# Performance work log

Hardware: AMD Instinct MI355X
Metric: run time of the kernel (lower is better)

Reference implementation:

```python
import jax, jax.numpy as jnp
import numpy as np

N_NODES = 100000
N_EDGES = 3200000
BATCH = 16
LAYER_NUMBER = 4


def setup_inputs() -> dict:
    key = jax.random.key(0)
    k1, k2, k3, k4 = jax.random.split(key, 4)
    x = jax.random.normal(k1, (N_NODES, BATCH), dtype=jnp.float32)
    # learnable per-edge weights (log1p(counts) at init in the original; the
    # parameter itself is what is learned, so a plain random init is faithful)
    weights = jax.random.normal(k2, (N_EDGES,), dtype=jnp.float32)
    row = jax.random.randint(k3, (N_EDGES,), 0, N_NODES, dtype=jnp.int64)
    col = jax.random.randint(k4, (N_EDGES,), 0, N_NODES, dtype=jnp.int64)
    return {"x": x, "weights": weights, "row": row, "col": col}


def reference(x, weights, row, col):
    # Repeated sparse COO SpMM: y <- A @ y, applied layer_number times,
    # where A[row[e], col[e]] = weights[e].
    def step(y, _):
        msg = weights[:, None] * y[col]                      # [E, B] gather + scale
        y_new = jax.ops.segment_sum(msg, row, num_segments=N_NODES)  # [N, B] scatter-add
        return y_new, None

    y, _ = jax.lax.scan(step, x, None, length=LAYER_NUMBER)
    return y
```

## Files before the change

### kernel.cpp

```cpp
#include <hip/hip_runtime.h>

#define N_NODES 100000
#define N_EDGES 3200000
#define BATCH 16
#define BKT_SHIFT 6
#define BKT_NODES 64
#define K_BUCKETS 1563
#define NB 256
#define SUB (N_EDGES / NB)
#define FT 512
#define SCAN_T 256
#define SCAN_C 7
#define CAP 4096

__global__ void hist_kernel(const int* __restrict__ row, int* __restrict__ blk_cnt) {
    __shared__ int lh[K_BUCKETS];
    int t = threadIdx.x, blk = blockIdx.x;
    for (int k = t; k < K_BUCKETS; k += 256) lh[k] = 0;
    __syncthreads();
    int base = blk * SUB;
    for (int e = base + t; e < base + SUB; e += 256)
        atomicAdd(&lh[row[e] >> BKT_SHIFT], 1);
    __syncthreads();
    for (int k = t; k < K_BUCKETS; k += 256)
        blk_cnt[k * NB + blk] = lh[k];
}

__global__ void colscan_kernel(int* __restrict__ blk_cnt, int* __restrict__ totals) {
    int bkt = blockIdx.x * blockDim.x + threadIdx.x;
    if (bkt >= K_BUCKETS) return;
    int4* p = (int4*)&blk_cnt[bkt * NB];
    int acc = 0;
    for (int q = 0; q < NB / 4; q++) {
        int4 v = p[q];
        int4 o;
        o.x = acc; acc += v.x;
        o.y = acc; acc += v.y;
        o.z = acc; acc += v.z;
        o.w = acc; acc += v.w;
        p[q] = o;
    }
    totals[bkt] = acc;
}

__global__ void scan_kernel(const int* __restrict__ totals, int* __restrict__ bptr,
                            int* __restrict__ row_ptr) {
    __shared__ int s[SCAN_T];
    int t = threadIdx.x;
    int loc[SCAN_C];
    int sum = 0;
    for (int i = 0; i < SCAN_C; i++) {
        int idx = t * SCAN_C + i;
        int v = (idx < K_BUCKETS) ? totals[idx] : 0;
        loc[i] = v;
        sum += v;
    }
    s[t] = sum;
    __syncthreads();
    for (int off = 1; off < SCAN_T; off <<= 1) {
        int x = (t >= off) ? s[t - off] : 0;
        __syncthreads();
        s[t] += x;
        __syncthreads();
    }
    int excl = s[t] - sum;
    for (int i = 0; i < SCAN_C; i++) {
        int idx = t * SCAN_C + i;
        if (idx < K_BUCKETS) bptr[idx] = excl;
        excl += loc[i];
    }
    if (t == 0) { bptr[K_BUCKETS] = N_EDGES; row_ptr[N_NODES] = N_EDGES; }
}

__global__ void __launch_bounds__(FT) fill_kernel(
        const int* __restrict__ row, const int* __restrict__ col,
        const float* __restrict__ w,
        const int* __restrict__ bptr, const int* __restrict__ blk_cnt,
        uint2* __restrict__ entries) {
    __shared__ uint2 sbuf[SUB];
    __shared__ int lbeg[K_BUCKETS];
    __shared__ int lcur[K_BUCKETS];
    __shared__ int sscan[FT];
    int t = threadIdx.x, blk = blockIdx.x;
    for (int k = t; k < K_BUCKETS; k += FT) lcur[k] = 0;
    __syncthreads();
    int base = blk * SUB;
    for (int e = base + t; e < base + SUB; e += FT)
        atomicAdd(&lcur[row[e] >> BKT_SHIFT], 1);
    __syncthreads();
    int loc[4];
    int sum = 0;
    #pragma unroll
    for (int j = 0; j < 4; j++) {
        int k = t * 4 + j;
        int v = (k < K_BUCKETS) ? lcur[k] : 0;
        loc[j] = v;
        sum += v;
    }
    sscan[t] = sum;
    __syncthreads();
    for (int off = 1; off < FT; off <<= 1) {
        int x = (t >= off) ? sscan[t - off] : 0;
        __syncthreads();
        sscan[t] += x;
        __syncthreads();
    }
    int excl = sscan[t] - sum;
    #pragma unroll
    for (int j = 0; j < 4; j++) {
        int k = t * 4 + j;
        if (k < K_BUCKETS) { lbeg[k] = excl; lcur[k] = excl; }
        excl += loc[j];
    }
    __syncthreads();
    for (int e = base + t; e < base + SUB; e += FT) {
        int r = row[e];
        int bkt = r >> BKT_SHIFT;
        int pos = atomicAdd(&lcur[bkt], 1);
        sbuf[pos] = make_uint2(((unsigned)(r & (BKT_NODES - 1)) << 17) | (unsigned)col[e],
                               __float_as_uint(w[e]));
    }
    __syncthreads();
    int lane = t & 7;
    for (int k = (t >> 3); k < K_BUCKETS; k += FT / 8) {
        int lb = lbeg[k];
        int le = lcur[k];
        int dst = bptr[k] + blk_cnt[k * NB + blk];
        for (int i = lb + lane; i < le; i += 8)
            entries[dst + (i - lb)] = sbuf[i];
    }
}

__global__ void nodesort_kernel(const int* __restrict__ bptr, uint2* __restrict__ entries,
                                int* __restrict__ row_ptr) {
    __shared__ uint2 ebuf[CAP];
    __shared__ int nh[BKT_NODES];
    __shared__ int nc[BKT_NODES];
    int t = threadIdx.x, b = blockIdx.x;
    int beg = bptr[b], end = bptr[b + 1];
    int n = min(end - beg, CAP);
    if (t < BKT_NODES) nh[t] = 0;
    __syncthreads();
    for (int k = t; k < n; k += 256) {
        uint2 r = entries[beg + k];
        ebuf[k] = r;
        atomicAdd(&nh[r.x >> 17], 1);
    }
    __syncthreads();
    if (t == 0) {
        int acc = 0;
        for (int i = 0; i < BKT_NODES; i++) {
            int v = nh[i];
            int node = b * BKT_NODES + i;
            if (node < N_NODES) row_ptr[node] = beg + acc;
            nc[i] = acc;
            acc += v;
        }
    }
    __syncthreads();
    for (int k = t; k < n; k += 256) {
        uint2 r = ebuf[k];
        int pos = atomicAdd(&nc[r.x >> 17], 1);
        entries[beg + pos] = r;
    }
}

__global__ void __launch_bounds__(256) pull_kernel(const float* __restrict__ y,
                            const uint2* __restrict__ entries,
                            const int* __restrict__ row_ptr,
                            float* __restrict__ out) {
    int tid = blockIdx.x * blockDim.x + threadIdx.x;
    int node = tid >> 2;
    int q = tid & 3;
    if (node >= N_NODES) return;
    int beg = row_ptr[node];
    int end = row_ptr[node + 1];
    float4 acc = make_float4(0.f, 0.f, 0.f, 0.f);
    if (beg < end) {
        int lim = end - 1;
        uint2 r[8];
        #pragma unroll
        for (int j = 0; j < 8; j++) r[j] = entries[min(beg + j, lim)];
        int i = beg;
        while (i + 8 <= end) {
            float4 yv[8];
            #pragma unroll
            for (int j = 0; j < 8; j++)
                yv[j] = *(const float4*)&y[(r[j].x & 0x1FFFFu) * BATCH + q * 4];
            uint2 nx[8];
            #pragma unroll
            for (int j = 0; j < 8; j++)
                nx[j] = entries[min(i + 8 + j, lim)];
            #pragma unroll
            for (int j = 0; j < 8; j++) {
                float wj = __uint_as_float(r[j].y);
                acc.x += wj * yv[j].x;
                acc.y += wj * yv[j].y;
                acc.z += wj * yv[j].z;
                acc.w += wj * yv[j].w;
            }
            #pragma unroll
            for (int j = 0; j < 8; j++) r[j] = nx[j];
            i += 8;
        }
        if (i < end) {
            float4 yv[8];
            #pragma unroll
            for (int j = 0; j < 8; j++)
                yv[j] = *(const float4*)&y[(r[j].x & 0x1FFFFu) * BATCH + q * 4];
            #pragma unroll
            for (int j = 0; j < 8; j++)
                if (i + j < end) {
                    float wj = __uint_as_float(r[j].y);
                    acc.x += wj * yv[j].x;
                    acc.y += wj * yv[j].y;
                    acc.z += wj * yv[j].z;
                    acc.w += wj * yv[j].w;
                }
        }
    }
    *(float4*)&out[node * BATCH + q * 4] = acc;
}

extern "C" void kernel_launch(void* const* d_in, const int* in_sizes, int n_in,
                              void* d_out, int out_size, void* d_ws, size_t ws_size,
                              hipStream_t stream) {
    const float* x   = (const float*)d_in[0];
    const float* w   = (const float*)d_in[1];
    const int*   row = (const int*)d_in[2];
    const int*   col = (const int*)d_in[3];
    float*       out = (float*)d_out;

    char* p = (char*)d_ws;
    uint2* entries = (uint2*)p;  p += (size_t)N_EDGES * sizeof(uint2);
    float* buf     = (float*)p;
    int*   blk_cnt = (int*)buf;
    p += (size_t)N_NODES * BATCH * sizeof(float);
    int* totals  = (int*)p;      p += 8192;
    int* bptr    = (int*)p;      p += 8192;
    int* row_ptr = (int*)p;

    hist_kernel<<<NB, 256, 0, stream>>>(row, blk_cnt);
    colscan_kernel<<<(K_BUCKETS + 255) / 256, 256, 0, stream>>>(blk_cnt, totals);
    scan_kernel<<<1, SCAN_T, 0, stream>>>(totals, bptr, row_ptr);
    fill_kernel<<<NB, FT, 0, stream>>>(row, col, w, bptr, blk_cnt, entries);
    nodesort_kernel<<<K_BUCKETS, 256, 0, stream>>>(bptr, entries, row_ptr);

    const int pgrid = (N_NODES * 4 + 255) / 256;
    pull_kernel<<<pgrid, 256, 0, stream>>>(x,   entries, row_ptr, buf);
    pull_kernel<<<pgrid, 256, 0, stream>>>(buf, entries, row_ptr, out);
    pull_kernel<<<pgrid, 256, 0, stream>>>(out, entries, row_ptr, buf);
    pull_kernel<<<pgrid, 256, 0, stream>>>(buf, entries, row_ptr, out);
}
```

Measured before the change: 357.9 us.

## Split feature batch into two half-width planes for cache-resident SpMM gathers

Adds a split kernel that rearranges x into two planar halves of 8 features each. Each layer then runs two pull passes, one per half, with 2 threads per node instead of 4. Halving the gathered vector table is meant to let the random y[col] gathers stay in on-chip cache. The cost is streaming the sorted edge entries twice per layer, plus one extra kernel launch per layer and a split pass; the last layer writes back in the interleaved output layout.

```diff
diff --git a/kernel.cpp b/kernel.cpp
--- a/kernel.cpp
+++ b/kernel.cpp
@@ -165,14 +165,28 @@
     }
 }
 
-__global__ void __launch_bounds__(256) pull_kernel(const float* __restrict__ y,
-                            const uint2* __restrict__ entries,
-                            const int* __restrict__ row_ptr,
-                            float* __restrict__ out) {
+__global__ void split_kernel(const float* __restrict__ x, float* __restrict__ planes) {
+    int node = blockIdx.x * blockDim.x + threadIdx.x;
+    if (node >= N_NODES) return;
+    const float4* src = (const float4*)&x[node * BATCH];
+    float4 a0 = src[0], a1 = src[1], a2 = src[2], a3 = src[3];
+    float4* p0 = (float4*)&planes[(size_t)node * 8];
+    p0[0] = a0; p0[1] = a1;
+    float4* p1 = (float4*)&planes[(size_t)N_NODES * 8 + (size_t)node * 8];
+    p1[0] = a2; p1[1] = a3;
+}
+
+__global__ void __launch_bounds__(256) pull_half_kernel(
+        const float* __restrict__ yplanes,
+        const uint2* __restrict__ entries,
+        const int* __restrict__ row_ptr,
+        float* __restrict__ out,
+        int half, int out_interleaved) {
     int tid = blockIdx.x * blockDim.x + threadIdx.x;
-    int node = tid >> 2;
-    int q = tid & 3;
+    int node = tid >> 1;
+    int q = tid & 1;
     if (node >= N_NODES) return;
+    const float* in = yplanes + (size_t)half * N_NODES * 8 + q * 4;
     int beg = row_ptr[node];
     int end = row_ptr[node + 1];
     float4 acc = make_float4(0.f, 0.f, 0.f, 0.f);
@@ -186,7 +200,7 @@
             float4 yv[8];
             #pragma unroll
             for (int j = 0; j < 8; j++)
-                yv[j] = *(const float4*)&y[(r[j].x & 0x1FFFFu) * BATCH + q * 4];
+                yv[j] = *(const float4*)&in[(r[j].x & 0x1FFFFu) * 8];
             uint2 nx[8];
             #pragma unroll
             for (int j = 0; j < 8; j++)
@@ -207,7 +221,7 @@
             float4 yv[8];
             #pragma unroll
             for (int j = 0; j < 8; j++)
-                yv[j] = *(const float4*)&y[(r[j].x & 0x1FFFFu) * BATCH + q * 4];
+                yv[j] = *(const float4*)&in[(r[j].x & 0x1FFFFu) * 8];
             #pragma unroll
             for (int j = 0; j < 8; j++)
                 if (i + j < end) {
@@ -219,7 +233,10 @@
                 }
         }
     }
-    *(float4*)&out[node * BATCH + q * 4] = acc;
+    size_t dst = out_interleaved
+        ? (size_t)node * BATCH + half * 8 + q * 4
+        : (size_t)half * N_NODES * 8 + (size_t)node * 8 + q * 4;
+    *(float4*)&out[dst] = acc;
 }
 
 extern "C" void kernel_launch(void* const* d_in, const int* in_sizes, int n_in,
@@ -246,9 +263,15 @@
     fill_kernel<<<NB, FT, 0, stream>>>(row, col, w, bptr, blk_cnt, entries);
     nodesort_kernel<<<K_BUCKETS, 256, 0, stream>>>(bptr, entries, row_ptr);
 
-    const int pgrid = (N_NODES * 4 + 255) / 256;
-    pull_kernel<<<pgrid, 256, 0, stream>>>(x,   entries, row_ptr, buf);
-    pull_kernel<<<pgrid, 256, 0, stream>>>(buf, entries, row_ptr, out);
-    pull_kernel<<<pgrid, 256, 0, stream>>>(out, entries, row_ptr, buf);
-    pull_kernel<<<pgrid, 256, 0, stream>>>(buf, entries, row_ptr, out);
-}
+    split_kernel<<<(N_NODES + 255) / 256, 256, 0, stream>>>(x, out);
+
+    const int pgrid = (N_NODES * 2 + 255) / 256;
+    pull_half_kernel<<<pgrid, 256, 0, stream>>>(out, entries, row_ptr, buf, 0, 0);
+    pull_half_kernel<<<pgrid, 256, 0, stream>>>(out, entries, row_ptr, buf, 1, 0);
+    pull_half_kernel<<<pgrid, 256, 0, stream>>>(buf, entries, row_ptr, out, 0, 0);
+    pull_half_kernel<<<pgrid, 256, 0, stream>>>(buf, entries, row_ptr, out, 1, 0);
+    pull_half_kernel<<<pgrid, 256, 0, stream>>>(out, entries, row_ptr, buf, 0, 0);
+    pull_half_kernel<<<pgrid, 256, 0, stream>>>(out, entries, row_ptr, buf, 1, 0);
+    pull_half_kernel<<<pgrid, 256, 0, stream>>>(buf, entries, row_ptr, out, 0, 1);
+    pull_half_kernel<<<pgrid, 256, 0, stream>>>(buf, entries, row_ptr, out, 1, 1);
+}
```

New measurement: 487.2 us. 36.1% more time.

## Double partition blocks and scan bucket counts with one wavefront per bucket

Applied to the files above, without the earlier changes.

Doubles the number of edge-partition blocks in the histogram and fill stages so each block handles half as many edges, giving more blocks to spread across CUs. The per-bucket column scan now uses a 64-lane wavefront with shuffle-based prefix sums instead of one serial thread per bucket, which matters more now that each column is twice as long. The fill copy-out uses 4 lanes per bucket instead of 8 to match the smaller per-bucket chunk sizes. The cost is a larger count matrix and more scattered, smaller copy segments.

```diff
diff --git a/kernel.cpp b/kernel.cpp
--- a/kernel.cpp
+++ b/kernel.cpp
@@ -6,7 +6,7 @@
 #define BKT_SHIFT 6
 #define BKT_NODES 64
 #define K_BUCKETS 1563
-#define NB 256
+#define NB 512
 #define SUB (N_EDGES / NB)
 #define FT 512
 #define SCAN_T 256
@@ -27,20 +27,33 @@
 }
 
 __global__ void colscan_kernel(int* __restrict__ blk_cnt, int* __restrict__ totals) {
-    int bkt = blockIdx.x * blockDim.x + threadIdx.x;
-    if (bkt >= K_BUCKETS) return;
-    int4* p = (int4*)&blk_cnt[bkt * NB];
-    int acc = 0;
-    for (int q = 0; q < NB / 4; q++) {
-        int4 v = p[q];
-        int4 o;
-        o.x = acc; acc += v.x;
-        o.y = acc; acc += v.y;
-        o.z = acc; acc += v.z;
-        o.w = acc; acc += v.w;
-        p[q] = o;
-    }
-    totals[bkt] = acc;
+    int wid = (blockIdx.x * blockDim.x + threadIdx.x) >> 6;
+    int lane = threadIdx.x & 63;
+    if (wid >= K_BUCKETS) return;
+    int* p = &blk_cnt[wid * NB + lane * 8];
+    int4 a = ((int4*)p)[0];
+    int4 b = ((int4*)p)[1];
+    int lt = a.x + a.y + a.z + a.w + b.x + b.y + b.z + b.w;
+    int pref = lt;
+    #pragma unroll
+    for (int off = 1; off < 64; off <<= 1) {
+        int v = __shfl_up(pref, off, 64);
+        if (lane >= off) pref += v;
+    }
+    int run = pref - lt;
+    int4 oa, ob;
+    oa.x = run; run += a.x;
+    oa.y = run; run += a.y;
+    oa.z = run; run += a.z;
+    oa.w = run; run += a.w;
+    ob.x = run; run += b.x;
+    ob.y = run; run += b.y;
+    ob.z = run; run += b.z;
+    ob.w = run; run += b.w;
+    ((int4*)p)[0] = oa;
+    ((int4*)p)[1] = ob;
+    int tot = __shfl(pref, 63, 64);
+    if (lane == 0) totals[wid] = tot;
 }
 
 __global__ void scan_kernel(const int* __restrict__ totals, int* __restrict__ bptr,
@@ -121,12 +134,12 @@
                                __float_as_uint(w[e]));
     }
     __syncthreads();
-    int lane = t & 7;
-    for (int k = (t >> 3); k < K_BUCKETS; k += FT / 8) {
+    int lane = t & 3;
+    for (int k = (t >> 2); k < K_BUCKETS; k += FT / 4) {
         int lb = lbeg[k];
         int le = lcur[k];
         int dst = bptr[k] + blk_cnt[k * NB + blk];
-        for (int i = lb + lane; i < le; i += 8)
+        for (int i = lb + lane; i < le; i += 4)
             entries[dst + (i - lb)] = sbuf[i];
     }
 }
@@ -241,7 +254,7 @@
     int* row_ptr = (int*)p;
 
     hist_kernel<<<NB, 256, 0, stream>>>(row, blk_cnt);
-    colscan_kernel<<<(K_BUCKETS + 255) / 256, 256, 0, stream>>>(blk_cnt, totals);
+    colscan_kernel<<<(K_BUCKETS * 64 + 255) / 256, 256, 0, stream>>>(blk_cnt, totals);
     scan_kernel<<<1, SCAN_T, 0, stream>>>(totals, bptr, row_ptr);
     fill_kernel<<<NB, FT, 0, stream>>>(row, col, w, bptr, blk_cnt, entries);
     nodesort_kernel<<<K_BUCKETS, 256, 0, stream>>>(bptr, entries, row_ptr);
```

New measurement: 329.6 us. 1.09x faster.
